# Kernel optimization log

Measured on AMD Instinct MI355X. Metric: run time of the kernel, lower is better.

The kernel has to match this reference:

```python
import jax, jax.numpy as jnp
import numpy as np

B, D = 4096, 128
LU, LI = 10, 20
NU, NI = 100000, 100000
NFU, NFI = 2000, 5000
MARGIN = 1.0


def setup_inputs() -> dict:
    key = jax.random.key(0)
    ks = jax.random.split(key, 32)
    s = 0.05
    n = lambda i, shape: (jax.random.normal(ks[i], shape, dtype=jnp.float32) * s)
    inp = {
        'user_indices': jax.random.randint(ks[0], (B,), 0, NU),
        'user_feat': jax.random.randint(ks[1], (B, LU), 0, NFU),
        'pos_item_indices': jax.random.randint(ks[2], (B,), 0, NI),
        'pos_item_feat': jax.random.randint(ks[3], (B, LI), 0, NFI),
        'neg_item_indices': jax.random.randint(ks[4], (B, 1), 0, NI),
        'neg_item_feat': jax.random.randint(ks[5], (B, 1, LI), 0, NFI),
        'comp_neg_indices': jax.random.randint(ks[6], (B,), 0, NI),
        'eps': jax.random.normal(ks[7], (B, D), dtype=jnp.float32),
        # learned parameters
        'emb_user': n(8, (NU, D)),
        'emb_item': n(9, (NI, D)),
        'emb_feat_user': n(10, (NFU, D)).at[0].set(0.0),  # row 0 is padding
        'emb_feat_item': n(11, (NFI, D)).at[0].set(0.0),
        'pop_emb_user': n(12, (D,)),
        'int_emb_user': n(13, (D,)),
        'pop_emb_item': n(14, (D,)),
        'int_emb_item': n(15, (D,)),
        'W_pop': n(16, (D, D)), 'b_pop': jnp.zeros((D,), jnp.float32),
        'W_int': n(17, (D, D)), 'b_int': jnp.zeros((D,), jnp.float32),
        'enc_W': n(18, (LI * D, D)), 'enc_b': jnp.zeros((D,), jnp.float32),
        'dec_W': n(19, (D, LI * D)), 'dec_b': jnp.zeros((LI * D,), jnp.float32),
        'fc11_W': n(20, (D, D)), 'fc11_b': jnp.zeros((D,), jnp.float32),
        'fc12_W': n(21, (D, D)), 'fc12_b': jnp.zeros((D,), jnp.float32),
    }
    return inp


def _attend_pool(fuse, feat_mask, vec, W, b):
    # fuse: [B, L+1, D], feat_mask: [B, L+1] (int, 0 = padded)
    scores = jnp.einsum('bld,d->bl', fuse, vec)
    scores = jnp.where(feat_mask == 0, -jnp.inf, scores)
    w = jax.nn.softmax(scores, axis=1)
    pooled = jnp.einsum('bld,bl->bd', fuse, w)
    return pooled @ W + b


def _branch(idx, feat, emb_table, feat_table, pop_vec, int_vec, W_pop, b_pop, W_int, b_int):
    e = emb_table[idx]                       # [B, D]
    fe = feat_table[feat]                    # [B, L, D]
    fuse = jnp.concatenate([e[:, None, :], fe], axis=1)           # [B, L+1, D]
    ones = jnp.ones((idx.shape[0], 1), dtype=feat.dtype)
    mask = jnp.concatenate([ones, feat], axis=1)                  # [B, L+1]
    hot = _attend_pool(fuse, mask, pop_vec, W_pop, b_pop)
    cold = _attend_pool(fuse, mask, int_vec, W_int, b_int)
    return hot, cold, e, fe


def reference(user_indices, user_feat, pos_item_indices, pos_item_feat,
              neg_item_indices, neg_item_feat, comp_neg_indices, eps,
              emb_user, emb_item, emb_feat_user, emb_feat_item,
              pop_emb_user, int_emb_user, pop_emb_item, int_emb_item,
              W_pop, b_pop, W_int, b_int,
              enc_W, enc_b, dec_W, dec_b, fc11_W, fc11_b, fc12_W, fc12_b):
    neg_item_indices = neg_item_indices.squeeze(1)
    neg_item_feat = neg_item_feat.squeeze(1)

    u_hot, u_cold, _, _ = _branch(user_indices, user_feat, emb_user, emb_feat_user,
                                  pop_emb_user, int_emb_user, W_pop, b_pop, W_int, b_int)
    p_hot, p_cold, pos_e, pos_fe = _branch(pos_item_indices, pos_item_feat, emb_item, emb_feat_item,
                                           pop_emb_item, int_emb_item, W_pop, b_pop, W_int, b_int)
    n_hot, n_cold, _, _ = _branch(neg_item_indices, neg_item_feat, emb_item, emb_feat_item,
                                  pop_emb_item, int_emb_item, W_pop, b_pop, W_int, b_int)

    loss_hot = jax.nn.relu(jnp.sum((u_hot - p_hot) ** 2, -1)
                           - jnp.sum((u_hot - n_hot) ** 2, -1) + MARGIN)
    loss_cold = jax.nn.relu(jnp.sum((u_cold - p_cold) ** 2, -1)
                            - jnp.sum((u_cold - n_cold) ** 2, -1) + MARGIN)

    # VAE over positive item feature embeddings
    x = pos_fe.reshape(pos_fe.shape[0], LI * D)
    h1 = jax.nn.relu(x @ enc_W + enc_b)
    mu = h1 @ fc11_W + fc11_b
    logvar = h1 @ fc12_W + fc12_b
    z = eps * jnp.exp(0.5 * logvar) + mu
    recon = z @ dec_W + dec_b                                    # [B, LI*D]
    mse = jnp.sum((recon - x) ** 2)
    kld = -0.5 * jnp.sum(1.0 + logvar - mu ** 2 - jnp.exp(logvar))
    vae_l = mse / LI + kld

    comp_e = emb_item[comp_neg_indices]
    mmi = -jnp.sum(jax.nn.log_sigmoid(jnp.sum(z * pos_e, 1) - jnp.sum(z * comp_e, 1)))
    item_vae_loss = mmi + vae_l + jnp.sum((z - pos_e) ** 2)

    return loss_hot, loss_cold, item_vae_loss
```

## Files before the change

### kernel.cpp

```cpp
#include <hip/hip_runtime.h>
#include <math.h>

#define BATCH 4096
#define DIM 128
#define LU 10
#define LI 20

typedef float  f32x4  __attribute__((ext_vector_type(4)));
typedef short  s16x8  __attribute__((ext_vector_type(8)));

__device__ __forceinline__ short f2bf(float x) {
    unsigned u = __float_as_uint(x);
    u += 0x7FFFu + ((u >> 16) & 1u);
    return (short)(u >> 16);
}

__global__ __launch_bounds__(256) void k_prep(
    const float* __restrict__ enc_W, const float* __restrict__ dec_W,
    const float* __restrict__ fc11_W, const float* __restrict__ fc12_W,
    const float* __restrict__ W_pop, const float* __restrict__ W_int,
    const float* __restrict__ ef_item, const float* __restrict__ ef_user,
    const float* __restrict__ pop_i, const float* __restrict__ int_i,
    const float* __restrict__ pop_u, const float* __restrict__ int_u,
    short* __restrict__ encWT, short* __restrict__ decWT,
    short* __restrict__ fc11WT, short* __restrict__ fc12WT,
    short* __restrict__ wpopT, short* __restrict__ wintT,
    short* __restrict__ ef16, short* __restrict__ efU16,
    float* __restrict__ projIP, float* __restrict__ projII,
    float* __restrict__ projUP, float* __restrict__ projUI)
{
    __shared__ float tile[32][33];
    const int b = blockIdx.x;
    const int t = threadIdx.x;

    if (b < 704) {
        const float* src; short* dst; int r0, c0, src_ld, dst_ld;
        if (b < 320) {
            int tk = b % 80, tj = b / 80;
            src = enc_W; dst = encWT; r0 = tk * 32; c0 = tj * 32; src_ld = 128; dst_ld = 2560;
        } else if (b < 640) {
            int tb = b - 320; int tc = tb % 80, td = tb / 80;
            src = dec_W; dst = decWT; r0 = td * 32; c0 = tc * 32; src_ld = 2560; dst_ld = 128;
        } else if (b < 656) {
            int tb = b - 640; int tk = tb % 4, tj = tb / 4;
            src = fc11_W; dst = fc11WT; r0 = tk * 32; c0 = tj * 32; src_ld = 128; dst_ld = 128;
        } else if (b < 672) {
            int tb = b - 656; int tk = tb % 4, tj = tb / 4;
            src = fc12_W; dst = fc12WT; r0 = tk * 32; c0 = tj * 32; src_ld = 128; dst_ld = 128;
        } else if (b < 688) {
            int tb = b - 672; int tk = tb % 4, tj = tb / 4;
            src = W_pop; dst = wpopT; r0 = tk * 32; c0 = tj * 32; src_ld = 128; dst_ld = 128;
        } else {
            int tb = b - 688; int tk = tb % 4, tj = tb / 4;
            src = W_int; dst = wintT; r0 = tk * 32; c0 = tj * 32; src_ld = 128; dst_ld = 128;
        }
        for (int q = 0; q < 4; ++q) {
            int e = t + q * 256;
            int r = e >> 5, c = e & 31;
            tile[r][c] = src[(size_t)(r0 + r) * src_ld + (c0 + c)];
        }
        __syncthreads();
        for (int q = 0; q < 4; ++q) {
            int e = t + q * 256;
            int r = e >> 5, c = e & 31;
            dst[(size_t)(c0 + r) * dst_ld + (r0 + c)] = f2bf(tile[c][r]);
        }
    } else if (b < 1329) {
        int base = (b - 704) * 1024 + t * 4;
        float4 v = *(const float4*)(ef_item + base);
        short4 o;
        o.x = f2bf(v.x); o.y = f2bf(v.y); o.z = f2bf(v.z); o.w = f2bf(v.w);
        *(short4*)(ef16 + base) = o;
    } else if (b < 1579) {
        int base = (b - 1329) * 1024 + t * 4;
        float4 v = *(const float4*)(ef_user + base);
        short4 o;
        o.x = f2bf(v.x); o.y = f2bf(v.y); o.z = f2bf(v.z); o.w = f2bf(v.w);
        *(short4*)(efU16 + base) = o;
    } else {
        const int pb = b - 1579;
        const float* tab; const float* v0p; const float* v1p;
        float* o0; float* o1; int row;
        if (pb < 625) {
            row = pb * 8 + (t >> 5);
            tab = ef_item; v0p = pop_i; v1p = int_i; o0 = projIP; o1 = projII;
        } else {
            row = (pb - 625) * 8 + (t >> 5);
            tab = ef_user; v0p = pop_u; v1p = int_u; o0 = projUP; o1 = projUI;
        }
        const int d = (t & 31) * 4;
        float4 rv = *(const float4*)(tab + (size_t)row * DIM + d);
        float4 a  = *(const float4*)(v0p + d);
        float4 c  = *(const float4*)(v1p + d);
        float s0 = rv.x * a.x + rv.y * a.y + rv.z * a.z + rv.w * a.w;
        float s1 = rv.x * c.x + rv.y * c.y + rv.z * c.z + rv.w * c.w;
        s0 += __shfl_xor(s0, 1, 64);  s1 += __shfl_xor(s1, 1, 64);
        s0 += __shfl_xor(s0, 2, 64);  s1 += __shfl_xor(s1, 2, 64);
        s0 += __shfl_xor(s0, 4, 64);  s1 += __shfl_xor(s1, 4, 64);
        s0 += __shfl_xor(s0, 8, 64);  s1 += __shfl_xor(s1, 8, 64);
        s0 += __shfl_xor(s0, 16, 64); s1 += __shfl_xor(s1, 16, 64);
        if ((t & 31) == 0) { o0[row] = s0; o1[row] = s1; }
    }
}

template<int L>
__device__ __forceinline__ void pool_sc(
    const int* __restrict__ idxp, const int* __restrict__ featp,
    const float* __restrict__ etab, const unsigned short* __restrict__ ftab16,
    const float* __restrict__ projP, const float* __restrict__ projI,
    const float* __restrict__ vpop, const float* __restrict__ vint,
    float* __restrict__ poolH, float* __restrict__ poolC,
    int i_in, int lane)
{
    const int i = __builtin_amdgcn_readfirstlane(i_in);
    const int d = lane * 2;

    int fidx[L];
#pragma unroll
    for (int l = 0; l < L; ++l) fidx[l] = featp[i * L + l];
    const int idx0 = idxp[i];

    const float2 e0 = *(const float2*)(etab + (size_t)idx0 * DIM + d);
    unsigned rr[L];
#pragma unroll
    for (int l = 0; l < L; ++l)
        rr[l] = *(const unsigned*)(ftab16 + (size_t)fidx[l] * DIM + d);

    float sp[L + 1], si[L + 1];
#pragma unroll
    for (int l = 0; l < L; ++l) {
        sp[l + 1] = projP[fidx[l]];
        si[l + 1] = projI[fidx[l]];
    }

    {
        const float2 vp = *(const float2*)(vpop + d);
        const float2 vi = *(const float2*)(vint + d);
        float aH = e0.x * vp.x + e0.y * vp.y;
        float aC = e0.x * vi.x + e0.y * vi.y;
        aH += __shfl_xor(aH, 1, 64);  aC += __shfl_xor(aC, 1, 64);
        aH += __shfl_xor(aH, 2, 64);  aC += __shfl_xor(aC, 2, 64);
        aH += __shfl_xor(aH, 4, 64);  aC += __shfl_xor(aC, 4, 64);
        aH += __shfl_xor(aH, 8, 64);  aC += __shfl_xor(aC, 8, 64);
        aH += __shfl_xor(aH, 16, 64); aC += __shfl_xor(aC, 16, 64);
        aH += __shfl_xor(aH, 32, 64); aC += __shfl_xor(aC, 32, 64);
        sp[0] = aH; si[0] = aC;
    }

    unsigned mbits = 1u;
#pragma unroll
    for (int l = 0; l < L; ++l) mbits |= (fidx[l] != 0 ? 2u : 0u) << l;

    float mh = sp[0], mc = si[0];
#pragma unroll
    for (int l = 1; l <= L; ++l) {
        bool v = (mbits >> l) & 1u;
        mh = v ? fmaxf(mh, sp[l]) : mh;
        mc = v ? fmaxf(mc, si[l]) : mc;
    }
    float sh = 0.f, sc = 0.f;
#pragma unroll
    for (int l = 0; l <= L; ++l) {
        bool v = (l == 0) | ((mbits >> l) & 1u);
        float eh = v ? __expf(sp[l] - mh) : 0.f;
        float ec = v ? __expf(si[l] - mc) : 0.f;
        sp[l] = eh; si[l] = ec;
        sh += eh; sc += ec;
    }
    const float rh = 1.f / sh, rc = 1.f / sc;

    float hx = sp[0] * e0.x, hy = sp[0] * e0.y;
    float cx = si[0] * e0.x, cy = si[0] * e0.y;
#pragma unroll
    for (int l = 0; l < L; ++l) {
        float x = __uint_as_float(rr[l] << 16);
        float y = __uint_as_float(rr[l] & 0xFFFF0000u);
        hx += sp[l + 1] * x; hy += sp[l + 1] * y;
        cx += si[l + 1] * x; cy += si[l + 1] * y;
    }
    float2 oH; oH.x = hx * rh; oH.y = hy * rh;
    float2 oC; oC.x = cx * rc; oC.y = cy * rc;
    *(float2*)(poolH + (size_t)i * DIM + d) = oH;
    *(float2*)(poolC + (size_t)i * DIM + d) = oC;
}

__global__ __launch_bounds__(512) void k_AB(
    const int* __restrict__ user_idx, const int* __restrict__ user_feat,
    const int* __restrict__ pos_idx,  const int* __restrict__ pos_feat,
    const int* __restrict__ neg_idx,  const int* __restrict__ neg_feat,
    const int* __restrict__ comp_idx,
    const float* __restrict__ emb_user, const float* __restrict__ emb_item,
    const float* __restrict__ ef_item,
    const float* __restrict__ pop_u, const float* __restrict__ int_u,
    const float* __restrict__ pop_i, const float* __restrict__ int_i,
    const float* __restrict__ eps,
    const float* __restrict__ enc_b, const float* __restrict__ dec_b,
    const float* __restrict__ fc11_b, const float* __restrict__ fc12_b,
    const short* __restrict__ encWT, const short* __restrict__ decWT,
    const short* __restrict__ fc11WT, const short* __restrict__ fc12WT,
    const short* __restrict__ ef16, const short* __restrict__ efU16,
    const float* __restrict__ projIP, const float* __restrict__ projII,
    const float* __restrict__ projUP, const float* __restrict__ projUI,
    float* __restrict__ pooled, float* __restrict__ vae_part)
{
    __shared__ int   featsL[320];
    __shared__ int   spi[16], sci[16];
    __shared__ __align__(16) short hlds[2048];
    __shared__ float xbuf[16][128];
    __shared__ float sdots[4][16][3];
    __shared__ float red[512];

    const int t    = threadIdx.x;
    const int w    = t >> 6;
    const int lane = t & 63;
    const int g    = lane >> 4;
    const int q    = lane & 15;
    const size_t SEC = (size_t)BATCH * DIM;

    if (blockIdx.x >= 256) {
        const int pb = blockIdx.x - 256;
        const int br = pb % 3;
        const int i  = (pb / 3) * 8 + w;
        if (br == 0) {
            pool_sc<LU>(user_idx, user_feat, emb_user,
                        (const unsigned short*)efU16, projUP, projUI,
                        pop_u, int_u,
                        pooled + 0 * SEC, pooled + 1 * SEC, i, lane);
        } else if (br == 1) {
            pool_sc<LI>(pos_idx, pos_feat, emb_item,
                        (const unsigned short*)ef16, projIP, projII,
                        pop_i, int_i,
                        pooled + 2 * SEC, pooled + 3 * SEC, i, lane);
        } else {
            pool_sc<LI>(neg_idx, neg_feat, emb_item,
                        (const unsigned short*)ef16, projIP, projII,
                        pop_i, int_i,
                        pooled + 4 * SEC, pooled + 5 * SEC, i, lane);
        }
        return;
    }

    const int i0   = blockIdx.x * 16;
    const int wcol = w & 3;
    const int wpar = w >> 2;

    if (t < 16)      spi[t] = pos_idx[i0 + t];
    else if (t < 32) sci[t - 16] = comp_idx[i0 + t - 16];
    if (t < 320) featsL[t] = pos_feat[i0 * LI + t];
    __syncthreads();

    const int j0 = wcol * 32 + q;
    const int j1 = j0 + 16;
    const short* bbase0 = encWT + (size_t)j0 * 2560 + g * 8;
    const short* bbase1 = encWT + (size_t)j1 * 2560 + g * 8;

    f32x4 acc0 = {0.f, 0.f, 0.f, 0.f};
    f32x4 acc1 = {0.f, 0.f, 0.f, 0.f};
    for (int l = wpar; l < LI; l += 2) {
        const int f = featsL[q * LI + l];
        const short* arow = ef16 + (size_t)f * DIM + g * 8;
#pragma unroll
        for (int dt = 0; dt < 4; ++dt) {
            const int koff = l * 128 + dt * 32;
            s16x8 a  = *(const s16x8*)(arow + dt * 32);
            s16x8 b0 = *(const s16x8*)(bbase0 + koff);
            s16x8 b1 = *(const s16x8*)(bbase1 + koff);
            acc0 = __builtin_amdgcn_mfma_f32_16x16x32_bf16(a, b0, acc0, 0, 0, 0);
            acc1 = __builtin_amdgcn_mfma_f32_16x16x32_bf16(a, b1, acc1, 0, 0, 0);
        }
    }

    if (wpar == 1) {
#pragma unroll
        for (int r = 0; r < 4; ++r) {
            int s = g * 4 + r;
            xbuf[s][j0] = acc0[r];
            xbuf[s][j1] = acc1[r];
        }
    }
    __syncthreads();
    if (wpar == 0) {
        float eb0 = enc_b[j0], eb1 = enc_b[j1];
#pragma unroll
        for (int r = 0; r < 4; ++r) {
            int s = g * 4 + r;
            float h0 = acc0[r] + xbuf[s][j0] + eb0; h0 = h0 > 0.f ? h0 : 0.f;
            float h1 = acc1[r] + xbuf[s][j1] + eb1; h1 = h1 > 0.f ? h1 : 0.f;
            int swz = (s & 7) << 3;
            hlds[(s * 128 + j0) ^ swz] = f2bf(h0);
            hlds[(s * 128 + j1) ^ swz] = f2bf(h1);
        }
    }
    __syncthreads();

    const short* WT  = (wpar == 0) ? fc11WT : fc12WT;
    const short* fb0 = WT + (size_t)j0 * DIM + g * 8;
    const short* fb1 = WT + (size_t)j1 * DIM + g * 8;
    f32x4 r0v = {0.f,0.f,0.f,0.f}, r1v = {0.f,0.f,0.f,0.f};
#pragma unroll
    for (int kt = 0; kt < 4; ++kt) {
        int sidx = (q * 128 + kt * 32 + g * 8) ^ ((q & 7) << 3);
        s16x8 a  = *(const s16x8*)&hlds[sidx];
        s16x8 w0 = *(const s16x8*)(fb0 + kt * 32);
        s16x8 w1 = *(const s16x8*)(fb1 + kt * 32);
        r0v = __builtin_amdgcn_mfma_f32_16x16x32_bf16(a, w0, r0v, 0, 0, 0);
        r1v = __builtin_amdgcn_mfma_f32_16x16x32_bf16(a, w1, r1v, 0, 0, 0);
    }
    if (wpar == 1) {
        float b12_0 = fc12_b[j0], b12_1 = fc12_b[j1];
#pragma unroll
        for (int r = 0; r < 4; ++r) {
            int s = g * 4 + r;
            xbuf[s][j0] = r0v[r] + b12_0;
            xbuf[s][j1] = r1v[r] + b12_1;
        }
    }
    __syncthreads();

    float kacc = 0.f;
    if (wpar == 0) {
        float b11_0 = fc11_b[j0], b11_1 = fc11_b[j1];
#pragma unroll
        for (int r = 0; r < 4; ++r) {
            const int s = g * 4 + r;
            const int i = i0 + s;
            float m0 = r0v[r] + b11_0, m1 = r1v[r] + b11_1;
            float v0 = xbuf[s][j0],  v1 = xbuf[s][j1];
            float e0 = eps[(size_t)i * DIM + j0];
            float e1 = eps[(size_t)i * DIM + j1];
            float z0 = e0 * expf(0.5f * v0) + m0;
            float z1 = e1 * expf(0.5f * v1) + m1;
            int swz = (s & 7) << 3;
            hlds[(s * 128 + j0) ^ swz] = f2bf(z0);
            hlds[(s * 128 + j1) ^ swz] = f2bf(z1);
            kacc += (1.f + v0 - m0 * m0 - expf(v0)) + (1.f + v1 - m1 * m1 - expf(v1));

            const size_t pb2 = (size_t)spi[s] * DIM;
            const size_t cb2 = (size_t)sci[s] * DIM;
            float pe0 = emb_item[pb2 + j0], pe1 = emb_item[pb2 + j1];
            float ce0 = emb_item[cb2 + j0], ce1 = emb_item[cb2 + j1];
            float zp = z0 * pe0 + z1 * pe1;
            float zc = z0 * ce0 + z1 * ce1;
            float d0 = z0 - pe0, d1 = z1 - pe1;
            float zq = d0 * d0 + d1 * d1;
            for (int mm = 8; mm >= 1; mm >>= 1) {
                zp += __shfl_xor(zp, mm, 64);
                zc += __shfl_xor(zc, mm, 64);
                zq += __shfl_xor(zq, mm, 64);
            }
            if (q == 0) {
                sdots[w][s][0] = zp;
                sdots[w][s][1] = zc;
                sdots[w][s][2] = zq;
            }
        }
    }
    __syncthreads();

    s16x8 za[4];
#pragma unroll
    for (int kt = 0; kt < 4; ++kt)
        za[kt] = *(const s16x8*)&hlds[(q * 128 + kt * 32 + g * 8) ^ ((q & 7) << 3)];

    const int cw = w * 320;
    float macc = 0.f;
    for (int fp = 0; fp < 10; ++fp) {
        const int c0 = cw + fp * 32 + q;
        const int c1 = c0 + 16;
        const short* bp0 = decWT + (size_t)c0 * DIM + g * 8;
        const short* bp1 = decWT + (size_t)c1 * DIM + g * 8;
        s16x8 b0[4], b1[4];
#pragma unroll
        for (int kt = 0; kt < 4; ++kt) {
            b0[kt] = *(const s16x8*)(bp0 + kt * 32);
            b1[kt] = *(const s16x8*)(bp1 + kt * 32);
        }
        const int l0 = c0 >> 7, d0 = c0 & 127;
        const int l1 = c1 >> 7, d1 = c1 & 127;
        float x0[4], x1[4];
#pragma unroll
        for (int r = 0; r < 4; ++r) {
            x0[r] = ef_item[(size_t)featsL[(g * 4 + r) * LI + l0] * DIM + d0];
            x1[r] = ef_item[(size_t)featsL[(g * 4 + r) * LI + l1] * DIM + d1];
        }
        const float bias0 = dec_b[c0], bias1 = dec_b[c1];
        f32x4 a0 = {0.f,0.f,0.f,0.f}, a1 = {0.f,0.f,0.f,0.f};
#pragma unroll
        for (int kt = 0; kt < 4; ++kt) {
            a0 = __builtin_amdgcn_mfma_f32_16x16x32_bf16(za[kt], b0[kt], a0, 0, 0, 0);
            a1 = __builtin_amdgcn_mfma_f32_16x16x32_bf16(za[kt], b1[kt], a1, 0, 0, 0);
        }
#pragma unroll
        for (int r = 0; r < 4; ++r) {
            float dd0 = a0[r] + bias0 - x0[r];
            float dd1 = a1[r] + bias1 - x1[r];
            macc += dd0 * dd0 + dd1 * dd1;
        }
    }

    red[t] = 0.05f * macc + ((wpar == 0) ? -0.5f * kacc : 0.f);
    __syncthreads();
    if (t < 16) {
        float zp = 0.f, zc = 0.f, zq = 0.f;
        for (int ww = 0; ww < 4; ++ww) {
            zp += sdots[ww][t][0];
            zc += sdots[ww][t][1];
            zq += sdots[ww][t][2];
        }
        float x = zp - zc;
        float ls = (x >= 0.f) ? -log1pf(expf(-x)) : (x - log1pf(expf(x)));
        red[t] += -ls + zq;
    }
    __syncthreads();
    for (int off = 256; off > 0; off >>= 1) {
        if (t < off) red[t] += red[t + off];
        __syncthreads();
    }
    if (t == 0) vae_part[blockIdx.x] = red[0];
}

__global__ __launch_bounds__(256) void k_loss(
    const float* __restrict__ pooled,
    const short* __restrict__ wpopT, const short* __restrict__ wintT,
    const float* __restrict__ vae_part,
    float* __restrict__ out_hot, float* __restrict__ out_cold,
    float* __restrict__ out_scalar)
{
    __shared__ float sArr[4][16];
    __shared__ float red[256];

    const int t    = threadIdx.x;
    const int w    = t >> 6;
    const int lane = t & 63;
    const int g    = lane >> 4;
    const int q    = lane & 15;
    const int i0   = blockIdx.x * 16;

    const int h     = w >> 1;
    const int other = (w & 1) + 1;
    const float* pu = pooled + (size_t)(0 * 2 + h) * BATCH * DIM;
    const float* po = pooled + (size_t)(other * 2 + h) * BATCH * DIM;
    const short* wT = h ? wintT : wpopT;

    s16x8 afr[4];
#pragma unroll
    for (int kt = 0; kt < 4; ++kt) {
        const size_t off = (size_t)(i0 + q) * DIM + kt * 32 + g * 8;
        f32x4 ua = *(const f32x4*)(pu + off);
        f32x4 ub = *(const f32x4*)(pu + off + 4);
        f32x4 oa = *(const f32x4*)(po + off);
        f32x4 ob = *(const f32x4*)(po + off + 4);
        s16x8 v;
        v[0] = f2bf(ua[0] - oa[0]); v[1] = f2bf(ua[1] - oa[1]);
        v[2] = f2bf(ua[2] - oa[2]); v[3] = f2bf(ua[3] - oa[3]);
        v[4] = f2bf(ub[0] - ob[0]); v[5] = f2bf(ub[1] - ob[1]);
        v[6] = f2bf(ub[2] - ob[2]); v[7] = f2bf(ub[3] - ob[3]);
        afr[kt] = v;
    }

    float sq0 = 0.f, sq1 = 0.f, sq2 = 0.f, sq3 = 0.f;
    for (int fr = 0; fr < 8; ++fr) {
        const short* bb = wT + (size_t)(fr * 16 + q) * DIM + g * 8;
        f32x4 acc = {0.f, 0.f, 0.f, 0.f};
#pragma unroll
        for (int kt = 0; kt < 4; ++kt) {
            s16x8 bfr = *(const s16x8*)(bb + kt * 32);
            acc = __builtin_amdgcn_mfma_f32_16x16x32_bf16(afr[kt], bfr, acc, 0, 0, 0);
        }
        sq0 += acc[0] * acc[0]; sq1 += acc[1] * acc[1];
        sq2 += acc[2] * acc[2]; sq3 += acc[3] * acc[3];
    }
    for (int m = 8; m >= 1; m >>= 1) {
        sq0 += __shfl_xor(sq0, m, 64);
        sq1 += __shfl_xor(sq1, m, 64);
        sq2 += __shfl_xor(sq2, m, 64);
        sq3 += __shfl_xor(sq3, m, 64);
    }
    if (q == 0) {
        sArr[w][g * 4 + 0] = sq0;
        sArr[w][g * 4 + 1] = sq1;
        sArr[w][g * 4 + 2] = sq2;
        sArr[w][g * 4 + 3] = sq3;
    }
    __syncthreads();
    if (t < 16) {
        float v = sArr[0][t] - sArr[1][t] + 1.0f;
        out_hot[i0 + t] = v > 0.f ? v : 0.f;
    } else if (t < 32) {
        int s = t - 16;
        float v = sArr[2][s] - sArr[3][s] + 1.0f;
        out_cold[i0 + s] = v > 0.f ? v : 0.f;
    }

    if (blockIdx.x == 0) {
        red[t] = vae_part[t];
        __syncthreads();
        for (int off = 128; off > 0; off >>= 1) {
            if (t < off) red[t] += red[t + off];
            __syncthreads();
        }
        if (t == 0) out_scalar[0] = red[0];
    }
}

extern "C" void kernel_launch(void* const* d_in, const int* in_sizes, int n_in,
                              void* d_out, int out_size, void* d_ws, size_t ws_size,
                              hipStream_t stream) {
    const int*   user_idx  = (const int*)d_in[0];
    const int*   user_feat = (const int*)d_in[1];
    const int*   pos_idx   = (const int*)d_in[2];
    const int*   pos_feat  = (const int*)d_in[3];
    const int*   neg_idx   = (const int*)d_in[4];
    const int*   neg_feat  = (const int*)d_in[5];
    const int*   comp_idx  = (const int*)d_in[6];
    const float* eps       = (const float*)d_in[7];
    const float* emb_user  = (const float*)d_in[8];
    const float* emb_item  = (const float*)d_in[9];
    const float* ef_user   = (const float*)d_in[10];
    const float* ef_item   = (const float*)d_in[11];
    const float* pop_u     = (const float*)d_in[12];
    const float* int_u     = (const float*)d_in[13];
    const float* pop_i     = (const float*)d_in[14];
    const float* int_i     = (const float*)d_in[15];
    const float* W_pop     = (const float*)d_in[16];
    const float* W_int     = (const float*)d_in[18];
    const float* enc_W     = (const float*)d_in[20];
    const float* enc_b     = (const float*)d_in[21];
    const float* dec_W     = (const float*)d_in[22];
    const float* dec_b     = (const float*)d_in[23];
    const float* fc11_W    = (const float*)d_in[24];
    const float* fc11_b    = (const float*)d_in[25];
    const float* fc12_W    = (const float*)d_in[26];
    const float* fc12_b    = (const float*)d_in[27];

    float* out = (float*)d_out;
    char*  ws  = (char*)d_ws;

    short* encWT    = (short*)(ws);
    short* decWT    = (short*)(ws + 655360);
    short* fc11WT   = (short*)(ws + 1310720);
    short* fc12WT   = (short*)(ws + 1343488);
    short* wpopT    = (short*)(ws + 1376256);
    short* wintT    = (short*)(ws + 1409024);
    short* ef16     = (short*)(ws + 1441792);
    short* efU16    = (short*)(ws + 2721792);
    float* pooled   = (float*)(ws + 4282368);
    float* vae_part = (float*)(ws + 16865280);
    float* projIP   = (float*)(ws + 16874496);
    float* projII   = (float*)(ws + 16894496);
    float* projUP   = (float*)(ws + 16914496);
    float* projUI   = (float*)(ws + 16922496);

    k_prep<<<dim3(2454), dim3(256), 0, stream>>>(
        enc_W, dec_W, fc11_W, fc12_W, W_pop, W_int, ef_item, ef_user,
        pop_i, int_i, pop_u, int_u,
        encWT, decWT, fc11WT, fc12WT, wpopT, wintT, ef16, efU16,
        projIP, projII, projUP, projUI);

    k_AB<<<dim3(1792), dim3(512), 0, stream>>>(
        user_idx, user_feat, pos_idx, pos_feat, neg_idx, neg_feat, comp_idx,
        emb_user, emb_item, ef_item,
        pop_u, int_u, pop_i, int_i,
        eps, enc_b, dec_b, fc11_b, fc12_b,
        encWT, decWT, fc11WT, fc12WT, ef16, efU16,
        projIP, projII, projUP, projUI,
        pooled, vae_part);

    k_loss<<<dim3(256), dim3(256), 0, stream>>>(
        pooled, wpopT, wintT, vae_part,
        out, out + BATCH, out + 2 * BATCH);
}
```

Before: 76.18 us.

## Split attention pooling into softmax-weight kernel and 16-lane-per-row pooling

The base-embedding score dot products move into extra k_prep blocks, and a new k_W kernel computes the softmax weights and reciprocal sums per sample, storing them in workspace. The pooling blocks in k_AB then use 16 lanes per row, each loading 8 bf16 features with uint4 loads, so four rows run per wave instead of one. The goal is to cut the cross-lane shuffle reductions and redundant per-lane score and softmax work, and to shrink the pooling grid. It adds a kernel launch and extra global traffic for the weight arrays, and k_W runs only 48 blocks of serial per-thread work.

```diff
diff --git a/kernel.cpp b/kernel.cpp
--- a/kernel.cpp
+++ b/kernel.cpp
@@ -5,6 +5,7 @@
 #define DIM 128
 #define LU 10
 #define LI 20
+#define NS 12288
 
 typedef float  f32x4  __attribute__((ext_vector_type(4)));
 typedef short  s16x8  __attribute__((ext_vector_type(8)));
@@ -22,12 +23,16 @@
     const float* __restrict__ ef_item, const float* __restrict__ ef_user,
     const float* __restrict__ pop_i, const float* __restrict__ int_i,
     const float* __restrict__ pop_u, const float* __restrict__ int_u,
+    const int* __restrict__ user_idx, const int* __restrict__ pos_idx,
+    const int* __restrict__ neg_idx,
+    const float* __restrict__ emb_user, const float* __restrict__ emb_item,
     short* __restrict__ encWT, short* __restrict__ decWT,
     short* __restrict__ fc11WT, short* __restrict__ fc12WT,
     short* __restrict__ wpopT, short* __restrict__ wintT,
     short* __restrict__ ef16, short* __restrict__ efU16,
     float* __restrict__ projIP, float* __restrict__ projII,
-    float* __restrict__ projUP, float* __restrict__ projUI)
+    float* __restrict__ projUP, float* __restrict__ projUI,
+    float* __restrict__ sEP, float* __restrict__ sEI)
 {
     __shared__ float tile[32][33];
     const int b = blockIdx.x;
@@ -77,7 +82,7 @@
         short4 o;
         o.x = f2bf(v.x); o.y = f2bf(v.y); o.z = f2bf(v.z); o.w = f2bf(v.w);
         *(short4*)(efU16 + base) = o;
-    } else {
+    } else if (b < 2454) {
         const int pb = b - 1579;
         const float* tab; const float* v0p; const float* v1p;
         float* o0; float* o1; int row;
@@ -100,88 +105,145 @@
         s0 += __shfl_xor(s0, 8, 64);  s1 += __shfl_xor(s1, 8, 64);
         s0 += __shfl_xor(s0, 16, 64); s1 += __shfl_xor(s1, 16, 64);
         if ((t & 31) == 0) { o0[row] = s0; o1[row] = s1; }
+    } else {
+        const int pb   = b - 2454;
+        const int wv   = pb * 4 + (t >> 6);
+        const int lane = t & 63;
+        const int g    = lane >> 3;
+        const int c    = lane & 7;
+        const int s    = wv * 8 + g;
+        const int br   = s >> 12;
+        const int i    = s & 4095;
+        const int* idxp   = (br == 0) ? user_idx : (br == 1 ? pos_idx : neg_idx);
+        const float* etab = (br == 0) ? emb_user : emb_item;
+        const float* vp   = (br == 0) ? pop_u : pop_i;
+        const float* vi   = (br == 0) ? int_u : int_i;
+        const int idx = idxp[i];
+        const float* rowp = etab + (size_t)idx * DIM + c * 16;
+        float sp = 0.f, si = 0.f;
+#pragma unroll
+        for (int j = 0; j < 4; ++j) {
+            float4 rv = *(const float4*)(rowp + j * 4);
+            float4 va = *(const float4*)(vp + c * 16 + j * 4);
+            float4 vb = *(const float4*)(vi + c * 16 + j * 4);
+            sp += rv.x * va.x + rv.y * va.y + rv.z * va.z + rv.w * va.w;
+            si += rv.x * vb.x + rv.y * vb.y + rv.z * vb.z + rv.w * vb.w;
+        }
+        sp += __shfl_xor(sp, 1, 64); si += __shfl_xor(si, 1, 64);
+        sp += __shfl_xor(sp, 2, 64); si += __shfl_xor(si, 2, 64);
+        sp += __shfl_xor(sp, 4, 64); si += __shfl_xor(si, 4, 64);
+        if (c == 0) { sEP[s] = sp; sEI[s] = si; }
     }
 }
 
 template<int L>
-__device__ __forceinline__ void pool_sc(
+__device__ __forceinline__ void w_one(
+    int s, int i, const int* __restrict__ featp,
+    const float* __restrict__ projP, const float* __restrict__ projI,
+    const float* __restrict__ sEP, const float* __restrict__ sEI,
+    float* __restrict__ wlP, float* __restrict__ wlI,
+    float* __restrict__ rinvH, float* __restrict__ rinvC)
+{
+    const float s0p = sEP[s], s0i = sEI[s];
+    float mh = s0p, mc = s0i;
+#pragma unroll
+    for (int l = 0; l < L; ++l) {
+        int f = featp[i * L + l];
+        if (f != 0) {
+            mh = fmaxf(mh, projP[f]);
+            mc = fmaxf(mc, projI[f]);
+        }
+    }
+    float sh = __expf(s0p - mh), sc = __expf(s0i - mc);
+    wlP[s] = sh;
+    wlI[s] = sc;
+#pragma unroll
+    for (int l = 0; l < L; ++l) {
+        int f = featp[i * L + l];
+        float eh = 0.f, ec = 0.f;
+        if (f != 0) {
+            eh = __expf(projP[f] - mh);
+            ec = __expf(projI[f] - mc);
+        }
+        wlP[(l + 1) * NS + s] = eh;
+        wlI[(l + 1) * NS + s] = ec;
+        sh += eh; sc += ec;
+    }
+    rinvH[s] = 1.f / sh;
+    rinvC[s] = 1.f / sc;
+}
+
+__global__ __launch_bounds__(256) void k_W(
+    const int* __restrict__ user_feat, const int* __restrict__ pos_feat,
+    const int* __restrict__ neg_feat,
+    const float* __restrict__ projIP, const float* __restrict__ projII,
+    const float* __restrict__ projUP, const float* __restrict__ projUI,
+    const float* __restrict__ sEP, const float* __restrict__ sEI,
+    float* __restrict__ wlP, float* __restrict__ wlI,
+    float* __restrict__ rinvH, float* __restrict__ rinvC)
+{
+    const int s = blockIdx.x * 256 + threadIdx.x;
+    const int i = s & 4095;
+    if (s < 4096) {
+        w_one<LU>(s, i, user_feat, projUP, projUI, sEP, sEI, wlP, wlI, rinvH, rinvC);
+    } else if (s < 8192) {
+        w_one<LI>(s, i, pos_feat, projIP, projII, sEP, sEI, wlP, wlI, rinvH, rinvC);
+    } else {
+        w_one<LI>(s, i, neg_feat, projIP, projII, sEP, sEI, wlP, wlI, rinvH, rinvC);
+    }
+}
+
+template<int L>
+__device__ __forceinline__ void pool_p(
     const int* __restrict__ idxp, const int* __restrict__ featp,
     const float* __restrict__ etab, const unsigned short* __restrict__ ftab16,
-    const float* __restrict__ projP, const float* __restrict__ projI,
-    const float* __restrict__ vpop, const float* __restrict__ vint,
+    const float* __restrict__ wlP, const float* __restrict__ wlI,
+    const float* __restrict__ rinvH, const float* __restrict__ rinvC,
     float* __restrict__ poolH, float* __restrict__ poolC,
-    int i_in, int lane)
+    int i, int sg, int c)
 {
-    const int i = __builtin_amdgcn_readfirstlane(i_in);
-    const int d = lane * 2;
-
-    int fidx[L];
-#pragma unroll
-    for (int l = 0; l < L; ++l) fidx[l] = featp[i * L + l];
-    const int idx0 = idxp[i];
-
-    const float2 e0 = *(const float2*)(etab + (size_t)idx0 * DIM + d);
-    unsigned rr[L];
-#pragma unroll
-    for (int l = 0; l < L; ++l)
-        rr[l] = *(const unsigned*)(ftab16 + (size_t)fidx[l] * DIM + d);
-
-    float sp[L + 1], si[L + 1];
+    const int d0 = c * 8;
+
+    float p0=0,p1=0,p2=0,p3=0,p4=0,p5=0,p6=0,p7=0;
+    float q0=0,q1=0,q2=0,q3=0,q4=0,q5=0,q6=0,q7=0;
+
+    {
+        const float* er = etab + (size_t)idxp[i] * DIM + d0;
+        float4 ea = *(const float4*)er;
+        float4 eb = *(const float4*)(er + 4);
+        float wp = wlP[sg], wi = wlI[sg];
+        p0 += wp*ea.x; p1 += wp*ea.y; p2 += wp*ea.z; p3 += wp*ea.w;
+        p4 += wp*eb.x; p5 += wp*eb.y; p6 += wp*eb.z; p7 += wp*eb.w;
+        q0 += wi*ea.x; q1 += wi*ea.y; q2 += wi*ea.z; q3 += wi*ea.w;
+        q4 += wi*eb.x; q5 += wi*eb.y; q6 += wi*eb.z; q7 += wi*eb.w;
+    }
+
 #pragma unroll
     for (int l = 0; l < L; ++l) {
-        sp[l + 1] = projP[fidx[l]];
-        si[l + 1] = projI[fidx[l]];
-    }
-
-    {
-        const float2 vp = *(const float2*)(vpop + d);
-        const float2 vi = *(const float2*)(vint + d);
-        float aH = e0.x * vp.x + e0.y * vp.y;
-        float aC = e0.x * vi.x + e0.y * vi.y;
-        aH += __shfl_xor(aH, 1, 64);  aC += __shfl_xor(aC, 1, 64);
-        aH += __shfl_xor(aH, 2, 64);  aC += __shfl_xor(aC, 2, 64);
-        aH += __shfl_xor(aH, 4, 64);  aC += __shfl_xor(aC, 4, 64);
-        aH += __shfl_xor(aH, 8, 64);  aC += __shfl_xor(aC, 8, 64);
-        aH += __shfl_xor(aH, 16, 64); aC += __shfl_xor(aC, 16, 64);
-        aH += __shfl_xor(aH, 32, 64); aC += __shfl_xor(aC, 32, 64);
-        sp[0] = aH; si[0] = aC;
-    }
-
-    unsigned mbits = 1u;
-#pragma unroll
-    for (int l = 0; l < L; ++l) mbits |= (fidx[l] != 0 ? 2u : 0u) << l;
-
-    float mh = sp[0], mc = si[0];
-#pragma unroll
-    for (int l = 1; l <= L; ++l) {
-        bool v = (mbits >> l) & 1u;
-        mh = v ? fmaxf(mh, sp[l]) : mh;
-        mc = v ? fmaxf(mc, si[l]) : mc;
-    }
-    float sh = 0.f, sc = 0.f;
-#pragma unroll
-    for (int l = 0; l <= L; ++l) {
-        bool v = (l == 0) | ((mbits >> l) & 1u);
-        float eh = v ? __expf(sp[l] - mh) : 0.f;
-        float ec = v ? __expf(si[l] - mc) : 0.f;
-        sp[l] = eh; si[l] = ec;
-        sh += eh; sc += ec;
-    }
-    const float rh = 1.f / sh, rc = 1.f / sc;
-
-    float hx = sp[0] * e0.x, hy = sp[0] * e0.y;
-    float cx = si[0] * e0.x, cy = si[0] * e0.y;
-#pragma unroll
-    for (int l = 0; l < L; ++l) {
-        float x = __uint_as_float(rr[l] << 16);
-        float y = __uint_as_float(rr[l] & 0xFFFF0000u);
-        hx += sp[l + 1] * x; hy += sp[l + 1] * y;
-        cx += si[l + 1] * x; cy += si[l + 1] * y;
-    }
-    float2 oH; oH.x = hx * rh; oH.y = hy * rh;
-    float2 oC; oC.x = cx * rc; oC.y = cy * rc;
-    *(float2*)(poolH + (size_t)i * DIM + d) = oH;
-    *(float2*)(poolC + (size_t)i * DIM + d) = oC;
+        const int f = featp[i * L + l];
+        const uint4 r = *(const uint4*)(ftab16 + (size_t)f * DIM + d0);
+        const float wp = wlP[(l + 1) * NS + sg];
+        const float wi = wlI[(l + 1) * NS + sg];
+        float x0 = __uint_as_float(r.x << 16), x1 = __uint_as_float(r.x & 0xFFFF0000u);
+        float x2 = __uint_as_float(r.y << 16), x3 = __uint_as_float(r.y & 0xFFFF0000u);
+        float x4 = __uint_as_float(r.z << 16), x5 = __uint_as_float(r.z & 0xFFFF0000u);
+        float x6 = __uint_as_float(r.w << 16), x7 = __uint_as_float(r.w & 0xFFFF0000u);
+        p0 += wp*x0; p1 += wp*x1; p2 += wp*x2; p3 += wp*x3;
+        p4 += wp*x4; p5 += wp*x5; p6 += wp*x6; p7 += wp*x7;
+        q0 += wi*x0; q1 += wi*x1; q2 += wi*x2; q3 += wi*x3;
+        q4 += wi*x4; q5 += wi*x5; q6 += wi*x6; q7 += wi*x7;
+    }
+
+    const float rh = rinvH[sg], rc = rinvC[sg];
+    float4 oa, ob;
+    oa.x = p0*rh; oa.y = p1*rh; oa.z = p2*rh; oa.w = p3*rh;
+    ob.x = p4*rh; ob.y = p5*rh; ob.z = p6*rh; ob.w = p7*rh;
+    *(float4*)(poolH + (size_t)i * DIM + d0)     = oa;
+    *(float4*)(poolH + (size_t)i * DIM + d0 + 4) = ob;
+    oa.x = q0*rc; oa.y = q1*rc; oa.z = q2*rc; oa.w = q3*rc;
+    ob.x = q4*rc; ob.y = q5*rc; ob.z = q6*rc; ob.w = q7*rc;
+    *(float4*)(poolC + (size_t)i * DIM + d0)     = oa;
+    *(float4*)(poolC + (size_t)i * DIM + d0 + 4) = ob;
 }
 
 __global__ __launch_bounds__(512) void k_AB(
@@ -191,16 +253,14 @@
     const int* __restrict__ comp_idx,
     const float* __restrict__ emb_user, const float* __restrict__ emb_item,
     const float* __restrict__ ef_item,
-    const float* __restrict__ pop_u, const float* __restrict__ int_u,
-    const float* __restrict__ pop_i, const float* __restrict__ int_i,
     const float* __restrict__ eps,
     const float* __restrict__ enc_b, const float* __restrict__ dec_b,
     const float* __restrict__ fc11_b, const float* __restrict__ fc12_b,
     const short* __restrict__ encWT, const short* __restrict__ decWT,
     const short* __restrict__ fc11WT, const short* __restrict__ fc12WT,
     const short* __restrict__ ef16, const short* __restrict__ efU16,
-    const float* __restrict__ projIP, const float* __restrict__ projII,
-    const float* __restrict__ projUP, const float* __restrict__ projUI,
+    const float* __restrict__ wlP, const float* __restrict__ wlI,
+    const float* __restrict__ rinvH, const float* __restrict__ rinvC,
     float* __restrict__ pooled, float* __restrict__ vae_part)
 {
     __shared__ int   featsL[320];
@@ -218,24 +278,23 @@
     const size_t SEC = (size_t)BATCH * DIM;
 
     if (blockIdx.x >= 256) {
-        const int pb = blockIdx.x - 256;
-        const int br = pb % 3;
-        const int i  = (pb / 3) * 8 + w;
+        const int p    = blockIdx.x - 256;
+        const int br   = p / 128;
+        const int i    = (p % 128) * 32 + w * 4 + (lane >> 4);
+        const int c    = lane & 15;
+        const int sg   = br * 4096 + i;
         if (br == 0) {
-            pool_sc<LU>(user_idx, user_feat, emb_user,
-                        (const unsigned short*)efU16, projUP, projUI,
-                        pop_u, int_u,
-                        pooled + 0 * SEC, pooled + 1 * SEC, i, lane);
+            pool_p<LU>(user_idx, user_feat, emb_user,
+                       (const unsigned short*)efU16, wlP, wlI, rinvH, rinvC,
+                       pooled + 0 * SEC, pooled + 1 * SEC, i, sg, c);
         } else if (br == 1) {
-            pool_sc<LI>(pos_idx, pos_feat, emb_item,
-                        (const unsigned short*)ef16, projIP, projII,
-                        pop_i, int_i,
-                        pooled + 2 * SEC, pooled + 3 * SEC, i, lane);
+            pool_p<LI>(pos_idx, pos_feat, emb_item,
+                       (const unsigned short*)ef16, wlP, wlI, rinvH, rinvC,
+                       pooled + 2 * SEC, pooled + 3 * SEC, i, sg, c);
         } else {
-            pool_sc<LI>(neg_idx, neg_feat, emb_item,
-                        (const unsigned short*)ef16, projIP, projII,
-                        pop_i, int_i,
-                        pooled + 4 * SEC, pooled + 5 * SEC, i, lane);
+            pool_p<LI>(neg_idx, neg_feat, emb_item,
+                       (const unsigned short*)ef16, wlP, wlI, rinvH, rinvC,
+                       pooled + 4 * SEC, pooled + 5 * SEC, i, sg, c);
         }
         return;
     }
@@ -550,20 +609,31 @@
     float* projII   = (float*)(ws + 16894496);
     float* projUP   = (float*)(ws + 16914496);
     float* projUI   = (float*)(ws + 16922496);
-
-    k_prep<<<dim3(2454), dim3(256), 0, stream>>>(
+    float* sEP      = (float*)(ws + 16930496);
+    float* sEI      = (float*)(ws + 16979648);
+    float* wlP      = (float*)(ws + 17028800);
+    float* wlI      = (float*)(ws + 18060992);
+    float* rinvH    = (float*)(ws + 19093184);
+    float* rinvC    = (float*)(ws + 19142336);
+
+    k_prep<<<dim3(2838), dim3(256), 0, stream>>>(
         enc_W, dec_W, fc11_W, fc12_W, W_pop, W_int, ef_item, ef_user,
         pop_i, int_i, pop_u, int_u,
+        user_idx, pos_idx, neg_idx, emb_user, emb_item,
         encWT, decWT, fc11WT, fc12WT, wpopT, wintT, ef16, efU16,
-        projIP, projII, projUP, projUI);
-
-    k_AB<<<dim3(1792), dim3(512), 0, stream>>>(
+        projIP, projII, projUP, projUI, sEP, sEI);
+
+    k_W<<<dim3(48), dim3(256), 0, stream>>>(
+        user_feat, pos_feat, neg_feat,
+        projIP, projII, projUP, projUI, sEP, sEI,
+        wlP, wlI, rinvH, rinvC);
+
+    k_AB<<<dim3(640), dim3(512), 0, stream>>>(
         user_idx, user_feat, pos_idx, pos_feat, neg_idx, neg_feat, comp_idx,
         emb_user, emb_item, ef_item,
-        pop_u, int_u, pop_i, int_i,
         eps, enc_b, dec_b, fc11_b, fc12_b,
         encWT, decWT, fc11WT, fc12WT, ef16, efU16,
-        projIP, projII, projUP, projUI,
+        wlP, wlI, rinvH, rinvC,
         pooled, vae_part);
 
     k_loss<<<dim3(256), dim3(256), 0, stream>>>(
```

New measurement: 94.17 us. +23.6%, slower.
